# Kernel tuning notes

Hardware: AMD Instinct MI355X
Metric: run time of the kernel (lower is better)

## Reference

```python
import jax, jax.numpy as jnp
import numpy as np

H_IMG = 256; W_IMG = 256; C = 256
WIN = (16, 16); STRIPE = (32, 32); DF = 4; NH = 4
ASZ = (STRIPE[0] // DF, STRIPE[1] // DF)
TS = ((STRIPE[0] + ASZ[0]) // 2, (STRIPE[1] + ASZ[1]) // 2)  # stripe bias table half-size (20,20)


def _win_part(x, ws):
    # (B,H,W,c) -> (B*nW, ws0*ws1, c)
    B, H, W, c = x.shape
    x = x.reshape(B, H // ws[0], ws[0], W // ws[1], ws[1], c)
    return x.transpose(0, 1, 3, 2, 4, 5).reshape(-1, ws[0] * ws[1], c)


def _win_rev(w, ws, H, W):
    c = w.shape[-1]
    B = w.shape[0] // ((H // ws[0]) * (W // ws[1]))
    x = w.reshape(B, H // ws[0], W // ws[1], ws[0], ws[1], c)
    return x.transpose(0, 1, 3, 2, 4, 5).reshape(B, H, W, c)


def _l2n(x):
    # F.normalize(dim=-1)
    return x / jnp.maximum(jnp.linalg.norm(x, axis=-1, keepdims=True), 1e-12)


def _affine(attn, logit_scale, w1, b1, w2, table, index):
    # attn: (B_, nH, N1, N2); AffineTransform with mask=None
    N1, N2 = attn.shape[-2], attn.shape[-1]
    attn = attn * jnp.exp(jnp.minimum(logit_scale, np.log(100.0)))  # clamp max=log(1/0.01)
    bt = jax.nn.relu(table.reshape(-1, 2) @ w1 + b1) @ w2  # (T, nH)
    bias = bt[index.reshape(-1)].reshape(N1, N2, -1).transpose(2, 0, 1)  # (nH,N1,N2)
    return attn + (16.0 * jax.nn.sigmoid(bias))[None]


def _coords(start, size):
    h = np.arange(start[0], start[0] + size[0])
    w = np.arange(start[1], start[1] + size[1])
    return np.stack(np.meshgrid(h, w, indexing='ij')).reshape(2, -1)


def _idx(c1, c2, md):
    d = (c1[:, :, None] - c2[:, None, :]).transpose(1, 2, 0).astype(np.int64)
    return (d[..., 0] + md[0] - 1) * (2 * md[1] - 1) + (d[..., 1] + md[1] - 1)


def _table(ts):
    h = np.arange(-(ts[0] - 1), ts[0], dtype=np.float32) / (ts[0] - 1)
    w = np.arange(-(ts[1] - 1), ts[1], dtype=np.float32) / (ts[1] - 1)
    t = np.stack(np.meshgrid(h, w, indexing='ij'), axis=-1)[None] * 8.0
    return (np.sign(t) * np.log2(np.abs(t) + 1.0) / np.log2(8.0)).astype(np.float32)


def setup_inputs():
    ks = iter(jax.random.split(jax.random.key(0), 32))
    def nrm(shape, s=0.02):
        return jax.random.normal(next(ks), shape, dtype=jnp.float32) * s
    inp = {}
    inp['x'] = jax.random.normal(next(ks), (1, H_IMG * W_IMG, C), dtype=jnp.float32)
    inp['qkv_w'] = nrm((C, 3 * C)); inp['qkv_b'] = nrm((3 * C,))
    inp['anchor_w'] = nrm((C, C // 2)); inp['anchor_b'] = nrm((C // 2,))
    for tag in ['w', 's1', 's2']:
        inp['ls_' + tag] = jnp.full((NH, 1, 1), np.log(10.0), dtype=jnp.float32)
        inp['cpb_w1_' + tag] = nrm((2, 512), 0.1)
        inp['cpb_b1_' + tag] = nrm((512,), 0.1)
        inp['cpb_w2_' + tag] = nrm((512, NH), 0.1)
    inp['proj_w'] = nrm((C, C)); inp['proj_b'] = nrm((C,))
    inp['table_w'] = jnp.asarray(_table(WIN))
    inp['table_s'] = jnp.asarray(_table(TS))
    cw = _coords((0, 0), WIN)
    inp['index_w'] = jnp.asarray(_idx(cw, cw, WIN), dtype=jnp.int32)
    cs = _coords((0, 0), STRIPE)
    st = ((STRIPE[0] - ASZ[0]) // 2, (STRIPE[1] - ASZ[1]) // 2)
    ca = _coords(st, ASZ)
    inp['index_a2w'] = jnp.asarray(_idx(ca, cs, TS), dtype=jnp.int32)
    inp['index_w2a'] = jnp.asarray(_idx(cs, ca, TS), dtype=jnp.int32)
    return inp


def reference(x, qkv_w, qkv_b, anchor_w, anchor_b,
              ls_w, cpb_w1_w, cpb_b1_w, cpb_w2_w,
              ls_s1, cpb_w1_s1, cpb_b1_s1, cpb_w2_s1,
              ls_s2, cpb_w1_s2, cpb_b1_s2, cpb_w2_s2,
              proj_w, proj_b, table_w, table_s,
              index_w, index_a2w, index_w2a):
    B, L, c = x.shape
    qkv = x @ qkv_w + qkv_b               # (B, L, 3C)
    half = 3 * c // 2
    hd = half // 3 // NH                  # head_dim per branch
    # ---- window attention on first half of qkv channels ----
    qw = _win_part(qkv[..., :half].reshape(B, H_IMG, W_IMG, half), WIN)  # (B_, N, 3*C/2)
    B_, N, _ = qw.shape
    q, k, v = qw.reshape(B_, N, 3, NH, hd).transpose(2, 0, 3, 1, 4)
    attn = jnp.einsum('bhnd,bhmd->bhnm', _l2n(q), _l2n(k))
    attn = jax.nn.softmax(_affine(attn, ls_w, cpb_w1_w, cpb_b1_w, cpb_w2_w, table_w, index_w), axis=-1)
    xw = jnp.einsum('bhnm,bhmd->bhnd', attn, v).transpose(0, 2, 1, 3).reshape(B_, N, NH * hd)
    xw = _win_rev(xw, WIN, H_IMG, W_IMG).reshape(B, L, c // 2)
    # ---- anchor projection: AvgPool2d(DF) + Linear(C -> C/2) ----
    xi = x.reshape(B, H_IMG, W_IMG, c)
    pooled = xi.reshape(B, H_IMG // DF, DF, W_IMG // DF, DF, c).mean(axis=(2, 4))
    anchor = pooled @ anchor_w + anchor_b  # (B, H/DF, W/DF, C/2)
    # ---- anchor stripe attention on second half ----
    qs = _win_part(qkv[..., half:].reshape(B, H_IMG, W_IMG, half), STRIPE)  # (Bs, N1, 3*C/2)
    Bs, N1, _ = qs.shape
    anc = _win_part(anchor, ASZ)           # (Bs, N2, C/2)
    N2 = anc.shape[1]
    q, k, v = qs.reshape(Bs, N1, 3, NH, hd).transpose(2, 0, 3, 1, 4)
    anc = anc.reshape(Bs, N2, NH, hd).transpose(0, 2, 1, 3)
    a1 = jnp.einsum('bhnd,bhmd->bhnm', _l2n(anc), _l2n(k))   # (Bs,NH,N2,N1)
    a1 = jax.nn.softmax(_affine(a1, ls_s1, cpb_w1_s1, cpb_b1_s1, cpb_w2_s1, table_s, index_a2w), axis=-1)
    xm = jnp.einsum('bhnm,bhmd->bhnd', a1, v)                # (Bs,NH,N2,hd)
    a2 = jnp.einsum('bhnd,bhmd->bhnm', _l2n(q), _l2n(anc))   # (Bs,NH,N1,N2)
    a2 = jax.nn.softmax(_affine(a2, ls_s2, cpb_w1_s2, cpb_b1_s2, cpb_w2_s2, table_s, index_w2a), axis=-1)
    xs = jnp.einsum('bhnm,bhmd->bhnd', a2, xm).transpose(0, 2, 1, 3).reshape(Bs, N1, NH * hd)
    xs = _win_rev(xs, STRIPE, H_IMG, W_IMG).reshape(B, L, c // 2)
    # ---- merge + output projection ----
    return jnp.concatenate([xw, xs], axis=-1) @ proj_w + proj_b
```

## Files before the change

### kernel.cpp

```cpp
#include <hip/hip_runtime.h>
#include <cstdint>
#include <cstddef>

typedef unsigned short u16;
typedef __attribute__((ext_vector_type(8))) short short8;
typedef __attribute__((ext_vector_type(4))) float floatx4;
typedef __attribute__((ext_vector_type(2))) float floatx2;
typedef __attribute__((ext_vector_type(4))) unsigned int uintx4;
typedef __attribute__((ext_vector_type(2))) unsigned int uintx2;
typedef __attribute__((ext_vector_type(2))) __bf16 bf16x2;

#define LOG2E 1.44269504f

__device__ __forceinline__ float bf2f(u16 u){
  union { unsigned int i; float f; } v; v.i = ((unsigned int)u) << 16; return v.f;
}
__device__ __forceinline__ u16 f2bf(float f){
  union { __bf16 b; u16 u; } v; v.b = (__bf16)f; return v.u;
}
__device__ __forceinline__ unsigned int pk2(float a, float b){
  union { bf16x2 h; unsigned int u; } v;
  v.h = __builtin_convertvector((floatx2){a, b}, bf16x2);
  return v.u;
}
__device__ __forceinline__ void gload16(const void* g, void* l){
  __builtin_amdgcn_global_load_lds((const __attribute__((address_space(1))) unsigned int*)g,
                                   (__attribute__((address_space(3))) unsigned int*)l, 16, 0, 0);
}
__device__ __forceinline__ uintx4 ld8f_bf(const float* g){
  floatx4 u0 = *(const floatx4*)g;
  floatx4 u1 = *(const floatx4*)(g + 4);
  uintx4 w;
  w.x = pk2(u0.x, u0.y); w.y = pk2(u0.z, u0.w);
  w.z = pk2(u1.x, u1.y); w.w = pk2(u1.z, u1.w);
  return w;
}
__device__ __forceinline__ float redq(float v){
  v += __shfl_xor(v, 16); v += __shfl_xor(v, 32);
  return v;
}

__global__ void transpose_w(const float* __restrict__ qkv_w, const float* __restrict__ anchor_w,
                            const float* __restrict__ proj_w,
                            u16* __restrict__ qkvt, u16* __restrict__ anct, u16* __restrict__ projt){
  int id = blockIdx.x*256 + threadIdx.x;
  if (id < 196608){ int k = id / 768, n = id % 768; qkvt[n*256 + k] = f2bf(qkv_w[id]); }
  else if (id < 229376){ int r = id - 196608; int k = r / 128, n = r % 128; anct[n*256 + k] = f2bf(anchor_w[r]); }
  else { int r = id - 229376; int k = r >> 8, n = r & 255; projt[n*256 + k] = f2bf(proj_w[r]); }
}

__global__ void cpb_mlp(const float* __restrict__ tw, const float* __restrict__ ts,
                        const float* __restrict__ w1w, const float* __restrict__ b1w, const float* __restrict__ w2w,
                        const float* __restrict__ w1s1, const float* __restrict__ b1s1, const float* __restrict__ w2s1,
                        const float* __restrict__ w1s2, const float* __restrict__ b1s2, const float* __restrict__ w2s2,
                        float* __restrict__ btw, float* __restrict__ bts1, float* __restrict__ bts2){
  int tag = blockIdx.y;
  const float *tab, *w1, *b1, *w2; float* bt; int T;
  if (tag == 0){ tab = tw; w1 = w1w;  b1 = b1w;  w2 = w2w;  bt = btw;  T = 961; }
  else if (tag == 1){ tab = ts; w1 = w1s1; b1 = b1s1; w2 = w2s1; bt = bts1; T = 1521; }
  else { tab = ts; w1 = w1s2; b1 = b1s2; w2 = w2s2; bt = bts2; T = 1521; }
  __shared__ float sw1[2][512];
  __shared__ float sb1[512];
  __shared__ float sw2[512][4];
  for (int j = threadIdx.x; j < 512; j += 256){
    sw1[0][j] = w1[j]; sw1[1][j] = w1[512 + j]; sb1[j] = b1[j];
    for (int h = 0; h < 4; ++h) sw2[j][h] = w2[j*4 + h];
  }
  __syncthreads();
  int idx = blockIdx.x*256 + threadIdx.x;
  int r = idx >> 2, hh = idx & 3;
  if (r < T){
    float t0 = tab[2*r], t1 = tab[2*r + 1];
    float acc = 0.f;
    for (int j = 0; j < 512; ++j){
      float hj = fmaxf(fmaf(t0, sw1[0][j], fmaf(t1, sw1[1][j], sb1[j])), 0.f);
      acc = fmaf(hj, sw2[j][hh], acc);
    }
    bt[r*4 + hh] = acc;
  }
}

__global__ void bias_gather(const float* __restrict__ btw, const float* __restrict__ bts1,
                            const float* __restrict__ bts2,
                            const int* __restrict__ idxw, const int* __restrict__ idxa2w,
                            const int* __restrict__ idxw2a,
                            const float* __restrict__ lsw, const float* __restrict__ ls1,
                            const float* __restrict__ ls2,
                            float* __restrict__ bw, float* __restrict__ bs1, float* __restrict__ bs2){
  int id = blockIdx.x*256 + threadIdx.x;
  int which = id >> 18;
  int rem = id & 262143;
  int h = rem >> 16, e = rem & 65535;
  const float* bt; const int* ix; float* dst; const float* ls;
  if (which == 0){ bt = btw;  ix = idxw;   dst = bw;  ls = lsw; }
  else if (which == 1){ bt = bts1; ix = idxa2w; dst = bs1; ls = ls1; }
  else { bt = bts2; ix = idxw2a; dst = bs2; ls = ls2; }
  float v = bt[ix[e]*4 + h];
  float scale = exp2f(fminf(ls[h], 4.6051702f) * LOG2E);
  float off = fminf(scale + 16.f, 80.f);
  float sig = 16.f / (1.f + exp2f(-v * LOG2E));
  float out = (sig - off) * LOG2E;
  int idx;
  if (which == 0){
    int q = e >> 8, k = e & 255;
    idx = ((((h*8 + (k>>5))*2 + ((k>>4)&1))*4 + ((k>>2)&3)) << 10) + (q << 2) + (k & 3);
  } else if (which == 1){
    int a = e >> 10, k = e & 1023;
    idx = (((h*64 + (k>>4))*4 + ((k>>2)&3)) << 8) + (a << 2) + (k & 3);
  } else {
    int q = e >> 6, k = e & 63;
    idx = (((h*4 + (k>>4))*4 + ((k>>2)&3)) << 12) + (q << 2) + (k & 3);
  }
  dst[idx] = out;
}

__global__ void avgpool(const float* __restrict__ x, float* __restrict__ pooled){
  int a = blockIdx.x, c = threadIdx.x;
  int ay = a >> 6, ax = a & 63;
  float acc = 0.f;
#pragma unroll
  for (int dy = 0; dy < 4; ++dy)
#pragma unroll
    for (int dx = 0; dx < 4; ++dx)
      acc += x[(size_t)((ay*4 + dy)*256 + ax*4 + dx)*256 + c];
  pooled[(size_t)a*256 + c] = acc * 0.0625f;
}

__launch_bounds__(256, 2)
__global__ void gemm_qkv(const float* __restrict__ A, const u16* __restrict__ Bt,
                         const float* __restrict__ bias, u16* __restrict__ C,
                         int N, int K){
  __shared__ __align__(16) u16 lsA[4096];
  __shared__ __align__(16) u16 lsB[4096];
  const int tid = threadIdx.x, lane = tid & 63, wv = tid >> 6;
  const int lane15 = lane & 15, quad = lane >> 4;
  const int wr = wv >> 1, wc = wv & 1;
  const int m0 = blockIdx.x * 128;
  const int y = blockIdx.y;
  const u16* Btb = Bt + (size_t)y*128*K;
  const float* bb = bias + y*128;
  char* lsBb = (char*)lsB;
  const int brow = wv*16 + (lane >> 2);
  const u16* bsrc = Btb + (size_t)brow*K + (lane & 3)*8;
  const int arow = tid & 127, aq = tid >> 7;
  const float* asrc = A + (size_t)(m0 + arow)*K;
  const int aslot0 = aq*1024 + ((arow + aq*2) & 127)*8;
  const int aslot1 = (aq+2)*1024 + ((arow + (aq+2)*2) & 127)*8;
  floatx4 acc[4][4] = {};
  for (int k0 = 0; k0 < K; k0 += 32){
    gload16(bsrc + k0,                 lsBb + wv*1024);
    gload16(bsrc + (size_t)64*K + k0,  lsBb + 4096 + wv*1024);
    uintx4 ra0 = ld8f_bf(asrc + k0 + aq*8);
    uintx4 ra1 = ld8f_bf(asrc + k0 + (aq+2)*8);
    *(uintx4*)(lsA + aslot0) = ra0;
    *(uintx4*)(lsA + aslot1) = ra1;
    __syncthreads();
    short8 a[4], b[4];
#pragma unroll
    for (int i = 0; i < 4; ++i){
      int r = wr*64 + i*16 + lane15;
      a[i] = *(const short8*)(lsA + quad*1024 + ((r + quad*2) & 127)*8);
    }
#pragma unroll
    for (int j = 0; j < 4; ++j)
      b[j] = *(const short8*)(lsBb + (wc*64 + j*16 + lane15)*64 + quad*16);
#pragma unroll
    for (int i = 0; i < 4; ++i)
#pragma unroll
      for (int j = 0; j < 4; ++j)
        acc[i][j] = __builtin_amdgcn_mfma_f32_16x16x32_bf16(b[j], a[i], acc[i][j], 0, 0, 0);
    __syncthreads();
  }
#pragma unroll
  for (int j = 0; j < 4; ++j){
    floatx4 bz = *(const floatx4*)(bb + wc*64 + j*16 + quad*4);
#pragma unroll
    for (int i = 0; i < 4; ++i) acc[i][j] += bz;
  }
  if (y < 2){
#pragma unroll
    for (int i = 0; i < 4; ++i){
#pragma unroll
      for (int jp = 0; jp < 2; ++jp){
        floatx4 s2 = acc[i][jp*2]*acc[i][jp*2] + acc[i][jp*2+1]*acc[i][jp*2+1];
        float ss = (s2.x + s2.y) + (s2.z + s2.w);
        ss = redq(ss);
        float inv = 1.f / fmaxf(sqrtf(ss), 1e-12f);
        acc[i][jp*2]   *= inv;
        acc[i][jp*2+1] *= inv;
      }
    }
  }
#pragma unroll
  for (int i = 0; i < 4; ++i){
    int row = m0 + wr*64 + i*16 + lane15;
#pragma unroll
    for (int j = 0; j < 4; ++j){
      int colb = y*128 + wc*64 + j*16 + quad*4;
      uintx2 w;
      w.x = pk2(acc[i][j][0], acc[i][j][1]);
      w.y = pk2(acc[i][j][2], acc[i][j][3]);
      *(uintx2*)(C + (size_t)row*N + colb) = w;
    }
  }
}

__launch_bounds__(256, 2)
__global__ void gemm_proj_inplace(float* __restrict__ AC, const u16* __restrict__ Bt,
                                  const float* __restrict__ bias){
  __shared__ __align__(16) u16 lsA[4096];
  __shared__ __align__(16) u16 lsB[8192];
  const int tid = threadIdx.x, lane = tid & 63, wv = tid >> 6;
  const int lane15 = lane & 15, quad = lane >> 4;
  const int wr = wv >> 1, wc = wv & 1;
  const int m0 = blockIdx.x * 128;
  char* lsBb = (char*)lsB;
  const int brow = wv*16 + (lane >> 2);
  const u16* bsrc = Bt + (size_t)brow*256 + (lane & 3)*8;
  const int arow = tid & 127, aq = tid >> 7;
  const float* asrc = AC + (size_t)(m0 + arow)*256;
  const int aslot0 = aq*1024 + ((arow + aq*2) & 127)*8;
  const int aslot1 = (aq+2)*1024 + ((arow + (aq+2)*2) & 127)*8;
  floatx4 acc[4][8] = {};
  for (int k0 = 0; k0 < 256; k0 += 32){
    gload16(bsrc + k0,                lsBb +         wv*1024);
    gload16(bsrc + 64*256 + k0,       lsBb + 4096  + wv*1024);
    gload16(bsrc + 128*256 + k0,      lsBb + 8192  + wv*1024);
    gload16(bsrc + 192*256 + k0,      lsBb + 12288 + wv*1024);
    uintx4 ra0 = ld8f_bf(asrc + k0 + aq*8);
    uintx4 ra1 = ld8f_bf(asrc + k0 + (aq+2)*8);
    *(uintx4*)(lsA + aslot0) = ra0;
    *(uintx4*)(lsA + aslot1) = ra1;
    __syncthreads();
    short8 a[4], b[8];
#pragma unroll
    for (int i = 0; i < 4; ++i){
      int r = wr*64 + i*16 + lane15;
      a[i] = *(const short8*)(lsA + quad*1024 + ((r + quad*2) & 127)*8);
    }
#pragma unroll
    for (int j = 0; j < 8; ++j)
      b[j] = *(const short8*)(lsBb + (wc*128 + j*16 + lane15)*64 + quad*16);
#pragma unroll
    for (int i = 0; i < 4; ++i)
#pragma unroll
      for (int j = 0; j < 8; ++j)
        acc[i][j] = __builtin_amdgcn_mfma_f32_16x16x32_bf16(b[j], a[i], acc[i][j], 0, 0, 0);
    __syncthreads();
  }
#pragma unroll
  for (int i = 0; i < 4; ++i){
    int row = m0 + wr*64 + i*16 + lane15;
#pragma unroll
    for (int j = 0; j < 8; ++j){
      int colb = wc*128 + j*16 + quad*4;
      floatx4 bz = *(const floatx4*)(bias + colb);
      floatx4 o = acc[i][j] + bz;
      *(floatx4*)(AC + (size_t)row*256 + colb) = o;
    }
  }
}

__launch_bounds__(256, 3)
__global__ void win_attn(const u16* __restrict__ qkvh, const float* __restrict__ lsw,
                         const float* __restrict__ biasw, float* __restrict__ outm, int r0){
  __shared__ __align__(16) u16 sm[24576];
  const int tid = threadIdx.x, lane = tid & 63, wv = tid >> 6;
  const int lane15 = lane & 15, quad = lane >> 4;
  const int h = blockIdx.y;
  const int wyl = blockIdx.x >> 4, wx = blockIdx.x & 15;
  u16* Ks = sm;
  u16* Qs = sm + 8192;
  u16* VT = sm + 16384;
  {
    int tok = wv*64 + lane;
    int row = (wyl*16 + (tok >> 4))*256 + wx*16 + (tok & 15);
    const char* src = (const char*)qkvh + (size_t)row*768 + h*64;
#pragma unroll
    for (int kq = 0; kq < 4; ++kq){
      gload16(src + kq*16,        (char*)Qs + wv*1024 + kq*4096);
      gload16(src + 256 + kq*16,  (char*)Ks + wv*1024 + kq*4096);
    }
    int vrow = (wyl*16 + (tid >> 4))*256 + wx*16 + (tid & 15);
    const uintx4* vp = (const uintx4*)((const char*)qkvh + (size_t)vrow*768 + 512 + h*64);
    uintx4 v0 = vp[0], v1 = vp[1], v2 = vp[2], v3 = vp[3];
    unsigned int w[16] = {v0.x,v0.y,v0.z,v0.w, v1.x,v1.y,v1.z,v1.w,
                          v2.x,v2.y,v2.z,v2.w, v3.x,v3.y,v3.z,v3.w};
    u16* vd = VT + (tid >> 3)*256 + (tid & 7);
#pragma unroll
    for (int c = 0; c < 16; ++c){
      vd[(c*2)*8]   = (u16)(w[c] & 0xffffu);
      vd[(c*2+1)*8] = (u16)(w[c] >> 16);
    }
  }
  __syncthreads();
  short8 qf[4];
#pragma unroll
  for (int j = 0; j < 4; ++j)
    qf[j] = *(const short8*)(Qs + quad*2048 + (wv*64 + j*16 + lane15)*8);
  __syncthreads();

  float scale = exp2f(fminf(lsw[h], 4.6051702f) * LOG2E) * LOG2E;
  u16* Pw = Qs + wv*2048;
  const floatx4 zf4 = {0.f, 0.f, 0.f, 0.f};
  floatx4 accO[2][4] = {};
  float lsum[4] = {};

  for (int kc = 0; kc < 8; ++kc){
    floatx4 bia[2][4];
#pragma unroll
    for (int i = 0; i < 2; ++i)
#pragma unroll
      for (int j = 0; j < 4; ++j)
        bia[i][j] = *(const floatx4*)(biasw + ((((h*8 + kc)*2 + i)*4 + quad) << 10)
                                            + ((wv*64 + j*16 + lane15) << 2));
    short8 kf[2];
#pragma unroll
    for (int i = 0; i < 2; ++i)
      kf[i] = *(const short8*)(Ks + quad*2048 + (kc*32 + i*16 + lane15)*8);
#pragma unroll
    for (int i = 0; i < 2; ++i)
#pragma unroll
      for (int j = 0; j < 4; ++j){
        floatx4 sv = __builtin_amdgcn_mfma_f32_16x16x32_bf16(kf[i], qf[j], zf4, 0, 0, 0);
        float p0 = exp2f(fmaf(sv[0], scale, bia[i][j][0]));
        float p1 = exp2f(fmaf(sv[1], scale, bia[i][j][1]));
        float p2 = exp2f(fmaf(sv[2], scale, bia[i][j][2]));
        float p3 = exp2f(fmaf(sv[3], scale, bia[i][j][3]));
        lsum[j] += (p0 + p1) + (p2 + p3);
        uintx2 w; w.x = pk2(p0, p1); w.y = pk2(p2, p3);
        *(uintx2*)(Pw + (i*2 + (quad>>1))*512 + (j*16 + lane15)*8 + (quad&1)*4) = w;
      }
    asm volatile("s_waitcnt lgkmcnt(0)" ::: "memory");
    short8 ptf[4], vtf[2];
#pragma unroll
    for (int j = 0; j < 4; ++j)
      ptf[j] = *(const short8*)(Pw + quad*512 + (j*16 + lane15)*8);
#pragma unroll
    for (int m = 0; m < 2; ++m)
      vtf[m] = *(const short8*)(VT + (kc*4 + quad)*256 + (m*16 + lane15)*8);
#pragma unroll
    for (int m = 0; m < 2; ++m)
#pragma unroll
      for (int j = 0; j < 4; ++j)
        accO[m][j] = __builtin_amdgcn_mfma_f32_16x16x32_bf16(vtf[m], ptf[j], accO[m][j], 0, 0, 0);
  }
  float linv[4];
#pragma unroll
  for (int j = 0; j < 4; ++j) linv[j] = 1.f / redq(lsum[j]);
#pragma unroll
  for (int m = 0; m < 2; ++m)
#pragma unroll
    for (int j = 0; j < 4; ++j){
      int tok = wv*64 + j*16 + lane15;
      int py = r0 + wyl*16 + (tok >> 4), px = wx*16 + (tok & 15);
      floatx4 o = accO[m][j] * linv[j];
      *(floatx4*)(outm + (size_t)(py*256 + px)*256 + h*32 + m*16 + quad*4) = o;
    }
}

__launch_bounds__(256, 3)
__global__ void stripe_xm(const u16* __restrict__ qkvh, const u16* __restrict__ anchor,
                          const float* __restrict__ ls1, const float* __restrict__ bias1,
                          float* __restrict__ gl1, u16* __restrict__ gO, int r0){
  __shared__ __align__(16) u16 sm[22528];
  const int tid = threadIdx.x, lane = tid & 63, wv = tid >> 6;
  const int lane15 = lane & 15, quad = lane >> 4;
  const int s = blockIdx.x, h = blockIdx.y, kb = blockIdx.z;
  const int syl = s >> 3, sx = s & 7;
  u16* ANC = sm; u16* VT = sm + 10240; u16* P1T = sm + 14336;
  if (wv == 0){
    int ay = (r0 >> 2) + syl*8 + (lane >> 3), ax = sx*8 + (lane & 7);
    const char* asrc = (const char*)anchor + (size_t)(ay*64 + ax)*256 + h*64;
#pragma unroll
    for (int kq = 0; kq < 4; ++kq)
      gload16(asrc + kq*16, (char*)ANC + kq*1024);
  }
  auto stageK = [&](int kc){
    int kkb = kb*512 + kc*128;
    char* KC = (char*)sm + 4096 + (kc & 1)*8192;
#pragma unroll
    for (int hf = 0; hf < 2; ++hf){
      int tok = kkb + hf*64 + lane;
      int row = (syl*32 + (tok >> 5))*256 + sx*32 + (tok & 31);
      gload16((const char*)qkvh + (size_t)row*768 + 256 + h*64 + wv*16,
              KC + wv*2048 + hf*1024);
    }
  };
  stageK(0);
  float scale1 = exp2f(fminf(ls1[h], 4.6051702f) * LOG2E) * LOG2E;
  const floatx4 zf4 = {0.f, 0.f, 0.f, 0.f};
  floatx4 accO1[2] = {};
  float l1 = 0.f;
  for (int kc = 0; kc < 4; ++kc){
    int kkb = kb*512 + kc*128;
    {
      int tok_l = tid >> 1, dh = tid & 1;
      int tok = kkb + tok_l;
      int row = (syl*32 + (tok >> 5))*256 + sx*32 + (tok & 31);
      const uintx4* vp = (const uintx4*)((const char*)qkvh + (size_t)row*768 + 512 + h*64 + dh*32);
      uintx4 v0 = vp[0], v1 = vp[1];
      unsigned int w[8] = {v0.x,v0.y,v0.z,v0.w, v1.x,v1.y,v1.z,v1.w};
      u16* vd = VT + (tok_l >> 3)*256 + dh*128 + (tok_l & 7);
#pragma unroll
      for (int c = 0; c < 8; ++c){
        vd[(c*2)*8]   = (u16)(w[c] & 0xffffu);
        vd[(c*2+1)*8] = (u16)(w[c] >> 16);
      }
    }
    __syncthreads();
    if (kc < 3) stageK(kc + 1);
    const u16* KC = sm + 2048 + (kc & 1)*4096;
    short8 ancf = *(const short8*)(ANC + quad*512 + (wv*16 + lane15)*8);
    floatx4 bia[8];
#pragma unroll
    for (int i = 0; i < 8; ++i)
      bia[i] = *(const floatx4*)(bias1 + (((h*64 + kb*32 + kc*8 + i)*4 + quad) << 8)
                                       + ((wv*16 + lane15) << 2));
#pragma unroll
    for (int i = 0; i < 8; ++i){
      short8 kf = *(const short8*)(KC + quad*1024 + (i*16 + lane15)*8);
      floatx4 sv = __builtin_amdgcn_mfma_f32_16x16x32_bf16(kf, ancf, zf4, 0, 0, 0);
      float p0 = exp2f(fmaf(sv[0], scale1, bia[i][0]));
      float p1 = exp2f(fmaf(sv[1], scale1, bia[i][1]));
      float p2 = exp2f(fmaf(sv[2], scale1, bia[i][2]));
      float p3 = exp2f(fmaf(sv[3], scale1, bia[i][3]));
      l1 += (p0 + p1) + (p2 + p3);
      uintx2 w; w.x = pk2(p0, p1); w.y = pk2(p2, p3);
      *(uintx2*)(P1T + (i*2 + (quad>>1))*512 + (wv*16 + lane15)*8 + (quad&1)*4) = w;
    }
    asm volatile("s_waitcnt lgkmcnt(0)" ::: "memory");
#pragma unroll
    for (int ks = 0; ks < 4; ++ks){
      short8 ptf = *(const short8*)(P1T + (ks*4 + quad)*512 + (wv*16 + lane15)*8);
#pragma unroll
      for (int m = 0; m < 2; ++m){
        short8 vtf = *(const short8*)(VT + (ks*4 + quad)*256 + (m*16 + lane15)*8);
        accO1[m] = __builtin_amdgcn_mfma_f32_16x16x32_bf16(vtf, ptf, accO1[m], 0, 0, 0);
      }
    }
    __syncthreads();
  }
  l1 = redq(l1);
  int ent = (s*4 + h)*2 + kb;
  if (quad == 0) gl1[ent*64 + wv*16 + lane15] = l1;
#pragma unroll
  for (int m = 0; m < 2; ++m){
    uintx2 w; w.x = pk2(accO1[m][0], accO1[m][1]); w.y = pk2(accO1[m][2], accO1[m][3]);
    *(uintx2*)(gO + (size_t)ent*2048 + (wv*16 + lane15)*32 + m*16 + quad*4) = w;
  }
}

__launch_bounds__(256, 3)
__global__ void stripe_xs(const u16* __restrict__ qkvh, const u16* __restrict__ anchor,
                          const float* __restrict__ ls2, const float* __restrict__ bias2,
                          const float* __restrict__ gl1, const u16* __restrict__ gO,
                          float* __restrict__ outm, int r0){
  __shared__ __align__(16) u16 sm[20480];
  const int tid = threadIdx.x, lane = tid & 63, wv = tid >> 6;
  const int lane15 = lane & 15, quad = lane >> 4;
  const int s = blockIdx.x >> 2, qc = blockIdx.x & 3, h = blockIdx.y;
  const int syl = s >> 3, sx = s & 7;
  u16* ANC = sm;
  u16* XMT = sm + 2048;
  u16* QW  = sm + 4096 + wv*2048;
  u16* P2T = sm + 12288 + wv*2048;
  if (wv == 0){
    int ay = (r0 >> 2) + syl*8 + (lane >> 3), ax = sx*8 + (lane & 7);
    const char* asrc = (const char*)anchor + (size_t)(ay*64 + ax)*256 + h*64;
#pragma unroll
    for (int kq = 0; kq < 4; ++kq)
      gload16(asrc + kq*16, (char*)ANC + kq*1024);
  }
  {
    int a = tid >> 2, db = (tid & 3)*8;
    int e0 = (s*4 + h)*2;
    float inv = 1.f / (gl1[e0*64 + a] + gl1[(e0 + 1)*64 + a]);
    uintx4 u0 = *(const uintx4*)(gO + (size_t)e0*2048 + a*32 + db);
    uintx4 u1 = *(const uintx4*)(gO + (size_t)(e0 + 1)*2048 + a*32 + db);
    unsigned int w0[4] = {u0.x, u0.y, u0.z, u0.w};
    unsigned int w1[4] = {u1.x, u1.y, u1.z, u1.w};
#pragma unroll
    for (int c = 0; c < 4; ++c){
      float a0 = bf2f((u16)(w0[c] & 0xffffu)) + bf2f((u16)(w1[c] & 0xffffu));
      float a1 = bf2f((u16)(w0[c] >> 16))     + bf2f((u16)(w1[c] >> 16));
      XMT[(a >> 3)*256 + (db + c*2)*8     + (a & 7)] = f2bf(a0 * inv);
      XMT[(a >> 3)*256 + (db + c*2 + 1)*8 + (a & 7)] = f2bf(a1 * inv);
    }
  }
  int tq = qc*256 + wv*64;
  {
    int tok = tq + lane;
    int row = (syl*32 + (tok >> 5))*256 + sx*32 + (tok & 31);
    const char* src = (const char*)qkvh + (size_t)row*768 + h*64;
#pragma unroll
    for (int kq = 0; kq < 4; ++kq)
      gload16(src + kq*16, (char*)QW + kq*1024);
  }
  __syncthreads();
  short8 qf2[4];
#pragma unroll
  for (int j = 0; j < 4; ++j)
    qf2[j] = *(const short8*)(QW + quad*512 + (j*16 + lane15)*8);
  float scale2 = exp2f(fminf(ls2[h], 4.6051702f) * LOG2E) * LOG2E;
  const floatx4 zf4 = {0.f, 0.f, 0.f, 0.f};
  floatx4 accO2[2][4] = {};
  float l2[4] = {};
#pragma unroll
  for (int c = 0; c < 2; ++c){
    floatx4 bia[2][4];
#pragma unroll
    for (int i = 0; i < 2; ++i)
#pragma unroll
      for (int j = 0; j < 4; ++j)
        bia[i][j] = *(const floatx4*)(bias2 + ((((h*4 + c*2 + i)*4 + quad) << 12)
                                             + ((tq + j*16 + lane15) << 2)));
    short8 af[2];
#pragma unroll
    for (int i = 0; i < 2; ++i)
      af[i] = *(const short8*)(ANC + quad*512 + (c*32 + i*16 + lane15)*8);
#pragma unroll
    for (int i = 0; i < 2; ++i)
#pragma unroll
      for (int j = 0; j < 4; ++j){
        floatx4 sv = __builtin_amdgcn_mfma_f32_16x16x32_bf16(af[i], qf2[j], zf4, 0, 0, 0);
        float p0 = exp2f(fmaf(sv[0], scale2, bia[i][j][0]));
        float p1 = exp2f(fmaf(sv[1], scale2, bia[i][j][1]));
        float p2 = exp2f(fmaf(sv[2], scale2, bia[i][j][2]));
        float p3 = exp2f(fmaf(sv[3], scale2, bia[i][j][3]));
        l2[j] += (p0 + p1) + (p2 + p3);
        uintx2 w; w.x = pk2(p0, p1); w.y = pk2(p2, p3);
        *(uintx2*)(P2T + (i*2 + (quad>>1))*512 + (j*16 + lane15)*8 + (quad&1)*4) = w;
      }
    asm volatile("s_waitcnt lgkmcnt(0)" ::: "memory");
    short8 ptf[4], xmf[2];
#pragma unroll
    for (int j = 0; j < 4; ++j)
      ptf[j] = *(const short8*)(P2T + quad*512 + (j*16 + lane15)*8);
#pragma unroll
    for (int m = 0; m < 2; ++m)
      xmf[m] = *(const short8*)(XMT + (c*4 + quad)*256 + (m*16 + lane15)*8);
#pragma unroll
    for (int m = 0; m < 2; ++m)
#pragma unroll
      for (int j = 0; j < 4; ++j)
        accO2[m][j] = __builtin_amdgcn_mfma_f32_16x16x32_bf16(xmf[m], ptf[j], accO2[m][j], 0, 0, 0);
  }
  float linv[4];
#pragma unroll
  for (int j = 0; j < 4; ++j) linv[j] = 1.f / redq(l2[j]);
#pragma unroll
  for (int m = 0; m < 2; ++m)
#pragma unroll
    for (int j = 0; j < 4; ++j){
      int tok = tq + j*16 + lane15;
      int py = r0 + syl*32 + (tok >> 5), px = sx*32 + (tok & 31);
      floatx4 o = accO2[m][j] * linv[j];
      *(floatx4*)(outm + (size_t)(py*256 + px)*256 + 128 + h*32 + m*16 + quad*4) = o;
    }
}

extern "C" void kernel_launch(void* const* d_in, const int* in_sizes, int n_in,
                              void* d_out, int out_size, void* d_ws, size_t ws_size,
                              hipStream_t stream) {
  (void)in_sizes; (void)n_in; (void)out_size; (void)ws_size;
  const float* x        = (const float*)d_in[0];
  const float* qkv_w    = (const float*)d_in[1];
  const float* qkv_b    = (const float*)d_in[2];
  const float* anchor_w = (const float*)d_in[3];
  const float* anchor_b = (const float*)d_in[4];
  const float* ls_w     = (const float*)d_in[5];
  const float* w1_w     = (const float*)d_in[6];
  const float* b1_w     = (const float*)d_in[7];
  const float* w2_w     = (const float*)d_in[8];
  const float* ls_s1    = (const float*)d_in[9];
  const float* w1_s1    = (const float*)d_in[10];
  const float* b1_s1    = (const float*)d_in[11];
  const float* w2_s1    = (const float*)d_in[12];
  const float* ls_s2    = (const float*)d_in[13];
  const float* w1_s2    = (const float*)d_in[14];
  const float* b1_s2    = (const float*)d_in[15];
  const float* w2_s2    = (const float*)d_in[16];
  const float* proj_w   = (const float*)d_in[17];
  const float* proj_b   = (const float*)d_in[18];
  const float* table_w  = (const float*)d_in[19];
  const float* table_s  = (const float*)d_in[20];
  const int* index_w   = (const int*)d_in[21];
  const int* index_a2w = (const int*)d_in[22];
  const int* index_w2a = (const int*)d_in[23];

  char* ws = (char*)d_ws;
  u16*   qkvh   = (u16*)(ws + 0);
  float* pooled = (float*)(ws + 0);
  u16*   anch   = (u16*)(ws + 25165824);
  u16*   qkvt   = (u16*)(ws + 26214400);
  u16*   anct   = (u16*)(ws + 26607616);
  u16*   projt  = (u16*)(ws + 26673152);
  float* btw    = (float*)(ws + 26804224);
  float* bts1   = (float*)(ws + 26820608);
  float* bts2   = (float*)(ws + 26845184);
  float* biasw  = (float*)(ws + 26869760);
  float* bias1  = (float*)(ws + 27918336);
  float* bias2  = (float*)(ws + 28966912);
  float* gl1    = (float*)(ws + 30015488);
  u16*   gO     = (u16*)(ws + 30081024);

  float* merged = (float*)d_out;

  transpose_w<<<1152, 256, 0, stream>>>(qkv_w, anchor_w, proj_w, qkvt, anct, projt);
  cpb_mlp<<<dim3(24, 3), 256, 0, stream>>>(table_w, table_s,
                                           w1_w, b1_w, w2_w,
                                           w1_s1, b1_s1, w2_s1,
                                           w1_s2, b1_s2, w2_s2,
                                           btw, bts1, bts2);
  bias_gather<<<3072, 256, 0, stream>>>(btw, bts1, bts2, index_w, index_a2w, index_w2a,
                                        ls_w, ls_s1, ls_s2, biasw, bias1, bias2);
  avgpool<<<4096, 256, 0, stream>>>(x, pooled);
  gemm_qkv<<<dim3(32, 1), 256, 0, stream>>>(pooled, anct, anchor_b, anch, 128, 256);

  for (int half = 0; half < 2; ++half){
    const float* xh = x + (size_t)half*32768*256;
    int r0 = half*128;
    gemm_qkv<<<dim3(256, 3), 256, 0, stream>>>(xh, qkvt, qkv_b, qkvh, 384, 256);
    win_attn<<<dim3(128, 4), 256, 0, stream>>>(qkvh, ls_w, biasw, merged, r0);
    gemm_qkv<<<dim3(256, 3), 256, 0, stream>>>(xh, qkvt + 384*256, qkv_b + 384, qkvh, 384, 256);
    stripe_xm<<<dim3(32, 4, 2), 256, 0, stream>>>(qkvh, anch, ls_s1, bias1, gl1, gO, r0);
    stripe_xs<<<dim3(128, 4), 256, 0, stream>>>(qkvh, anch, ls_s2, bias2, gl1, gO, merged, r0);
  }

  gemm_proj_inplace<<<dim3(512), 256, 0, stream>>>(merged, projt, proj_b);
}
```

Measured before the change: 396.6 us.

## Fuse QKV column tiles per block, drop half-split, store merged bf16

The QKV GEMM now has each block stage its 128-row fp32 A tile once into LDS as bf16 and loop over all three 128-column output tiles, with double-buffered B loads. This removes the repeated A reads and conversions across blockIdx.y. The two image halves are processed in single full-size launches using separate workspace buffers for the window and stripe QKV. Attention outputs are written to a bf16 merged buffer, which the projection GEMM reads with async double-buffered loads instead of converting fp32 in place. The cost is more LDS per block (64KB for A), which may lower occupancy, plus a larger workspace footprint.

```diff
diff --git a/kernel.cpp b/kernel.cpp
--- a/kernel.cpp
+++ b/kernel.cpp
@@ -127,126 +127,133 @@
 }
 
 __launch_bounds__(256, 2)
-__global__ void gemm_qkv(const float* __restrict__ A, const u16* __restrict__ Bt,
-                         const float* __restrict__ bias, u16* __restrict__ C,
-                         int N, int K){
-  __shared__ __align__(16) u16 lsA[4096];
-  __shared__ __align__(16) u16 lsB[4096];
+__global__ void gemm_fused(const float* __restrict__ A, const u16* __restrict__ Bt,
+                           const float* __restrict__ bias, u16* __restrict__ C,
+                           int NY, int normY){
+  __shared__ __align__(16) u16 lsA[32768];
+  __shared__ __align__(16) u16 lsB[2][4096];
   const int tid = threadIdx.x, lane = tid & 63, wv = tid >> 6;
   const int lane15 = lane & 15, quad = lane >> 4;
   const int wr = wv >> 1, wc = wv & 1;
   const int m0 = blockIdx.x * 128;
-  const int y = blockIdx.y;
-  const u16* Btb = Bt + (size_t)y*128*K;
-  const float* bb = bias + y*128;
-  char* lsBb = (char*)lsB;
+  const int N = NY * 128;
   const int brow = wv*16 + (lane >> 2);
-  const u16* bsrc = Btb + (size_t)brow*K + (lane & 3)*8;
-  const int arow = tid & 127, aq = tid >> 7;
-  const float* asrc = A + (size_t)(m0 + arow)*K;
-  const int aslot0 = aq*1024 + ((arow + aq*2) & 127)*8;
-  const int aslot1 = (aq+2)*1024 + ((arow + (aq+2)*2) & 127)*8;
-  floatx4 acc[4][4] = {};
-  for (int k0 = 0; k0 < K; k0 += 32){
-    gload16(bsrc + k0,                 lsBb + wv*1024);
-    gload16(bsrc + (size_t)64*K + k0,  lsBb + 4096 + wv*1024);
-    uintx4 ra0 = ld8f_bf(asrc + k0 + aq*8);
-    uintx4 ra1 = ld8f_bf(asrc + k0 + (aq+2)*8);
-    *(uintx4*)(lsA + aslot0) = ra0;
-    *(uintx4*)(lsA + aslot1) = ra1;
-    __syncthreads();
-    short8 a[4], b[4];
+  const int bk = (lane & 3)*8;
+  auto stageB = [&](int y, int kw, int buf){
+    const u16* bs = Bt + (size_t)(y*128 + brow)*256 + kw*32 + bk;
+    char* d = (char*)lsB[buf];
+    gload16(bs,            d + wv*1024);
+    gload16(bs + 64*256,   d + 4096 + wv*1024);
+  };
+  stageB(0, 0, 0);
+  {
+    const int row = tid & 127, kh = tid >> 7;
+    const float* ap = A + (size_t)(m0 + row)*256 + kh*128;
+#pragma unroll
+    for (int i = 0; i < 16; ++i){
+      int k8 = kh*16 + i;
+      uintx4 w = ld8f_bf(ap + i*8);
+      *(uintx4*)(lsA + ((size_t)k8*128 + ((row + k8*2) & 127))*8) = w;
+    }
+  }
+  for (int y = 0; y < NY; ++y){
+    floatx4 acc[4][4] = {};
+    for (int kw = 0; kw < 8; ++kw){
+      const int it = y*8 + kw;
+      __syncthreads();
+      if (it + 1 < NY*8){
+        int nit = it + 1;
+        stageB(nit >> 3, nit & 7, nit & 1);
+      }
+      const char* Bc = (const char*)lsB[it & 1];
+      const int k8 = kw*4 + quad;
+      short8 a[4], b[4];
+#pragma unroll
+      for (int i = 0; i < 4; ++i)
+        a[i] = *(const short8*)(lsA + ((size_t)k8*128 + ((wr*64 + i*16 + lane15 + k8*2) & 127))*8);
+#pragma unroll
+      for (int j = 0; j < 4; ++j)
+        b[j] = *(const short8*)(Bc + (wc*64 + j*16 + lane15)*64 + quad*16);
+#pragma unroll
+      for (int i = 0; i < 4; ++i)
+#pragma unroll
+        for (int j = 0; j < 4; ++j)
+          acc[i][j] = __builtin_amdgcn_mfma_f32_16x16x32_bf16(b[j], a[i], acc[i][j], 0, 0, 0);
+    }
+#pragma unroll
+    for (int j = 0; j < 4; ++j){
+      floatx4 bz = *(const floatx4*)(bias + y*128 + wc*64 + j*16 + quad*4);
+#pragma unroll
+      for (int i = 0; i < 4; ++i) acc[i][j] += bz;
+    }
+    if (y < normY){
+#pragma unroll
+      for (int i = 0; i < 4; ++i)
+#pragma unroll
+        for (int jp = 0; jp < 2; ++jp){
+          floatx4 s2 = acc[i][jp*2]*acc[i][jp*2] + acc[i][jp*2+1]*acc[i][jp*2+1];
+          float ss = (s2.x + s2.y) + (s2.z + s2.w);
+          ss = redq(ss);
+          float inv = 1.f / fmaxf(sqrtf(ss), 1e-12f);
+          acc[i][jp*2]   *= inv;
+          acc[i][jp*2+1] *= inv;
+        }
+    }
 #pragma unroll
     for (int i = 0; i < 4; ++i){
-      int r = wr*64 + i*16 + lane15;
-      a[i] = *(const short8*)(lsA + quad*1024 + ((r + quad*2) & 127)*8);
-    }
-#pragma unroll
-    for (int j = 0; j < 4; ++j)
-      b[j] = *(const short8*)(lsBb + (wc*64 + j*16 + lane15)*64 + quad*16);
-#pragma unroll
-    for (int i = 0; i < 4; ++i)
-#pragma unroll
-      for (int j = 0; j < 4; ++j)
-        acc[i][j] = __builtin_amdgcn_mfma_f32_16x16x32_bf16(b[j], a[i], acc[i][j], 0, 0, 0);
-    __syncthreads();
-  }
-#pragma unroll
-  for (int j = 0; j < 4; ++j){
-    floatx4 bz = *(const floatx4*)(bb + wc*64 + j*16 + quad*4);
-#pragma unroll
-    for (int i = 0; i < 4; ++i) acc[i][j] += bz;
-  }
-  if (y < 2){
-#pragma unroll
-    for (int i = 0; i < 4; ++i){
-#pragma unroll
-      for (int jp = 0; jp < 2; ++jp){
-        floatx4 s2 = acc[i][jp*2]*acc[i][jp*2] + acc[i][jp*2+1]*acc[i][jp*2+1];
-        float ss = (s2.x + s2.y) + (s2.z + s2.w);
-        ss = redq(ss);
-        float inv = 1.f / fmaxf(sqrtf(ss), 1e-12f);
-        acc[i][jp*2]   *= inv;
-        acc[i][jp*2+1] *= inv;
+      int row = m0 + wr*64 + i*16 + lane15;
+#pragma unroll
+      for (int j = 0; j < 4; ++j){
+        int colb = y*128 + wc*64 + j*16 + quad*4;
+        uintx2 w;
+        w.x = pk2(acc[i][j][0], acc[i][j][1]);
+        w.y = pk2(acc[i][j][2], acc[i][j][3]);
+        *(uintx2*)(C + (size_t)row*N + colb) = w;
       }
     }
   }
-#pragma unroll
-  for (int i = 0; i < 4; ++i){
-    int row = m0 + wr*64 + i*16 + lane15;
-#pragma unroll
-    for (int j = 0; j < 4; ++j){
-      int colb = y*128 + wc*64 + j*16 + quad*4;
-      uintx2 w;
-      w.x = pk2(acc[i][j][0], acc[i][j][1]);
-      w.y = pk2(acc[i][j][2], acc[i][j][3]);
-      *(uintx2*)(C + (size_t)row*N + colb) = w;
-    }
-  }
 }
 
 __launch_bounds__(256, 2)
-__global__ void gemm_proj_inplace(float* __restrict__ AC, const u16* __restrict__ Bt,
-                                  const float* __restrict__ bias){
-  __shared__ __align__(16) u16 lsA[4096];
-  __shared__ __align__(16) u16 lsB[8192];
+__global__ void gemm_proj(const u16* __restrict__ Ab, const u16* __restrict__ Bt,
+                          const float* __restrict__ bias, float* __restrict__ Cout){
+  __shared__ __align__(16) u16 lsA[2][4096];
+  __shared__ __align__(16) u16 lsB[2][8192];
   const int tid = threadIdx.x, lane = tid & 63, wv = tid >> 6;
   const int lane15 = lane & 15, quad = lane >> 4;
   const int wr = wv >> 1, wc = wv & 1;
   const int m0 = blockIdx.x * 128;
-  char* lsBb = (char*)lsB;
-  const int brow = wv*16 + (lane >> 2);
-  const u16* bsrc = Bt + (size_t)brow*256 + (lane & 3)*8;
-  const int arow = tid & 127, aq = tid >> 7;
-  const float* asrc = AC + (size_t)(m0 + arow)*256;
-  const int aslot0 = aq*1024 + ((arow + aq*2) & 127)*8;
-  const int aslot1 = (aq+2)*1024 + ((arow + (aq+2)*2) & 127)*8;
+  const int srow = wv*16 + (lane >> 2), sk = (lane & 3)*8;
+  const u16* as = Ab + (size_t)(m0 + srow)*256 + sk;
+  const u16* bs = Bt + (size_t)srow*256 + sk;
+  auto stage = [&](int kw, int buf){
+    char* dA = (char*)lsA[buf]; char* dB = (char*)lsB[buf];
+    gload16(as + kw*32,             dA + wv*1024);
+    gload16(as + 64*256 + kw*32,    dA + 4096  + wv*1024);
+    gload16(bs + kw*32,             dB + wv*1024);
+    gload16(bs + 64*256 + kw*32,    dB + 4096  + wv*1024);
+    gload16(bs + 128*256 + kw*32,   dB + 8192  + wv*1024);
+    gload16(bs + 192*256 + kw*32,   dB + 12288 + wv*1024);
+  };
+  stage(0, 0);
   floatx4 acc[4][8] = {};
-  for (int k0 = 0; k0 < 256; k0 += 32){
-    gload16(bsrc + k0,                lsBb +         wv*1024);
-    gload16(bsrc + 64*256 + k0,       lsBb + 4096  + wv*1024);
-    gload16(bsrc + 128*256 + k0,      lsBb + 8192  + wv*1024);
-    gload16(bsrc + 192*256 + k0,      lsBb + 12288 + wv*1024);
-    uintx4 ra0 = ld8f_bf(asrc + k0 + aq*8);
-    uintx4 ra1 = ld8f_bf(asrc + k0 + (aq+2)*8);
-    *(uintx4*)(lsA + aslot0) = ra0;
-    *(uintx4*)(lsA + aslot1) = ra1;
+  for (int kw = 0; kw < 8; ++kw){
     __syncthreads();
+    if (kw < 7) stage(kw + 1, (kw + 1) & 1);
+    const char* Ac = (const char*)lsA[kw & 1];
+    const char* Bc = (const char*)lsB[kw & 1];
     short8 a[4], b[8];
 #pragma unroll
-    for (int i = 0; i < 4; ++i){
-      int r = wr*64 + i*16 + lane15;
-      a[i] = *(const short8*)(lsA + quad*1024 + ((r + quad*2) & 127)*8);
-    }
+    for (int i = 0; i < 4; ++i)
+      a[i] = *(const short8*)(Ac + (wr*64 + i*16 + lane15)*64 + quad*16);
 #pragma unroll
     for (int j = 0; j < 8; ++j)
-      b[j] = *(const short8*)(lsBb + (wc*128 + j*16 + lane15)*64 + quad*16);
+      b[j] = *(const short8*)(Bc + (wc*128 + j*16 + lane15)*64 + quad*16);
 #pragma unroll
     for (int i = 0; i < 4; ++i)
 #pragma unroll
       for (int j = 0; j < 8; ++j)
         acc[i][j] = __builtin_amdgcn_mfma_f32_16x16x32_bf16(b[j], a[i], acc[i][j], 0, 0, 0);
-    __syncthreads();
   }
 #pragma unroll
   for (int i = 0; i < 4; ++i){
@@ -256,14 +263,14 @@
       int colb = wc*128 + j*16 + quad*4;
       floatx4 bz = *(const floatx4*)(bias + colb);
       floatx4 o = acc[i][j] + bz;
-      *(floatx4*)(AC + (size_t)row*256 + colb) = o;
+      *(floatx4*)(Cout + (size_t)row*256 + colb) = o;
     }
   }
 }
 
 __launch_bounds__(256, 3)
 __global__ void win_attn(const u16* __restrict__ qkvh, const float* __restrict__ lsw,
-                         const float* __restrict__ biasw, float* __restrict__ outm, int r0){
+                         const float* __restrict__ biasw, u16* __restrict__ outm){
   __shared__ __align__(16) u16 sm[24576];
   const int tid = threadIdx.x, lane = tid & 63, wv = tid >> 6;
   const int lane15 = lane & 15, quad = lane >> 4;
@@ -353,16 +360,17 @@
 #pragma unroll
     for (int j = 0; j < 4; ++j){
       int tok = wv*64 + j*16 + lane15;
-      int py = r0 + wyl*16 + (tok >> 4), px = wx*16 + (tok & 15);
+      int py = wyl*16 + (tok >> 4), px = wx*16 + (tok & 15);
       floatx4 o = accO[m][j] * linv[j];
-      *(floatx4*)(outm + (size_t)(py*256 + px)*256 + h*32 + m*16 + quad*4) = o;
+      uintx2 w; w.x = pk2(o[0], o[1]); w.y = pk2(o[2], o[3]);
+      *(uintx2*)(outm + (size_t)(py*256 + px)*256 + h*32 + m*16 + quad*4) = w;
     }
 }
 
 __launch_bounds__(256, 3)
 __global__ void stripe_xm(const u16* __restrict__ qkvh, const u16* __restrict__ anchor,
                           const float* __restrict__ ls1, const float* __restrict__ bias1,
-                          float* __restrict__ gl1, u16* __restrict__ gO, int r0){
+                          float* __restrict__ gl1, u16* __restrict__ gO){
   __shared__ __align__(16) u16 sm[22528];
   const int tid = threadIdx.x, lane = tid & 63, wv = tid >> 6;
   const int lane15 = lane & 15, quad = lane >> 4;
@@ -370,7 +378,7 @@
   const int syl = s >> 3, sx = s & 7;
   u16* ANC = sm; u16* VT = sm + 10240; u16* P1T = sm + 14336;
   if (wv == 0){
-    int ay = (r0 >> 2) + syl*8 + (lane >> 3), ax = sx*8 + (lane & 7);
+    int ay = syl*8 + (lane >> 3), ax = sx*8 + (lane & 7);
     const char* asrc = (const char*)anchor + (size_t)(ay*64 + ax)*256 + h*64;
 #pragma unroll
     for (int kq = 0; kq < 4; ++kq)
@@ -455,7 +463,7 @@
 __global__ void stripe_xs(const u16* __restrict__ qkvh, const u16* __restrict__ anchor,
                           const float* __restrict__ ls2, const float* __restrict__ bias2,
                           const float* __restrict__ gl1, const u16* __restrict__ gO,
-                          float* __restrict__ outm, int r0){
+                          u16* __restrict__ outm){
   __shared__ __align__(16) u16 sm[20480];
   const int tid = threadIdx.x, lane = tid & 63, wv = tid >> 6;
   const int lane15 = lane & 15, quad = lane >> 4;
@@ -466,7 +474,7 @@
   u16* QW  = sm + 4096 + wv*2048;
   u16* P2T = sm + 12288 + wv*2048;
   if (wv == 0){
-    int ay = (r0 >> 2) + syl*8 + (lane >> 3), ax = sx*8 + (lane & 7);
+    int ay = syl*8 + (lane >> 3), ax = sx*8 + (lane & 7);
     const char* asrc = (const char*)anchor + (size_t)(ay*64 + ax)*256 + h*64;
 #pragma unroll
     for (int kq = 0; kq < 4; ++kq)
@@ -554,9 +562,10 @@
 #pragma unroll
     for (int j = 0; j < 4; ++j){
       int tok = tq + j*16 + lane15;
-      int py = r0 + syl*32 + (tok >> 5), px = sx*32 + (tok & 31);
+      int py = syl*32 + (tok >> 5), px = sx*32 + (tok & 31);
       floatx4 o = accO2[m][j] * linv[j];
-      *(floatx4*)(outm + (size_t)(py*256 + px)*256 + 128 + h*32 + m*16 + quad*4) = o;
+      uintx2 w; w.x = pk2(o[0], o[1]); w.y = pk2(o[2], o[3]);
+      *(uintx2*)(outm + (size_t)(py*256 + px)*256 + 128 + h*32 + m*16 + quad*4) = w;
     }
 }
 
@@ -590,22 +599,22 @@
   const int* index_w2a = (const int*)d_in[23];
 
   char* ws = (char*)d_ws;
-  u16*   qkvh   = (u16*)(ws + 0);
-  float* pooled = (float*)(ws + 0);
-  u16*   anch   = (u16*)(ws + 25165824);
-  u16*   qkvt   = (u16*)(ws + 26214400);
-  u16*   anct   = (u16*)(ws + 26607616);
-  u16*   projt  = (u16*)(ws + 26673152);
-  float* btw    = (float*)(ws + 26804224);
-  float* bts1   = (float*)(ws + 26820608);
-  float* bts2   = (float*)(ws + 26845184);
-  float* biasw  = (float*)(ws + 26869760);
-  float* bias1  = (float*)(ws + 27918336);
-  float* bias2  = (float*)(ws + 28966912);
-  float* gl1    = (float*)(ws + 30015488);
-  u16*   gO     = (u16*)(ws + 30081024);
-
-  float* merged = (float*)d_out;
+  u16*   qkvhW  = (u16*)(ws + 0);
+  u16*   qkvhS  = (u16*)(ws + 50331648);
+  u16*   mergedb= (u16*)(ws + 100663296);
+  float* pooled = (float*)(ws + 134217728);
+  u16*   anch   = (u16*)(ws + 138412032);
+  u16*   qkvt   = (u16*)(ws + 139460608);
+  u16*   anct   = (u16*)(ws + 139853824);
+  u16*   projt  = (u16*)(ws + 139919360);
+  float* btw    = (float*)(ws + 140050432);
+  float* bts1   = (float*)(ws + 140066816);
+  float* bts2   = (float*)(ws + 140091392);
+  float* biasw  = (float*)(ws + 140115968);
+  float* bias1  = (float*)(ws + 141164544);
+  float* bias2  = (float*)(ws + 142213120);
+  float* gl1    = (float*)(ws + 143261696);
+  u16*   gO     = (u16*)(ws + 143392768);
 
   transpose_w<<<1152, 256, 0, stream>>>(qkv_w, anchor_w, proj_w, qkvt, anct, projt);
   cpb_mlp<<<dim3(24, 3), 256, 0, stream>>>(table_w, table_s,
@@ -616,17 +625,11 @@
   bias_gather<<<3072, 256, 0, stream>>>(btw, bts1, bts2, index_w, index_a2w, index_w2a,
                                         ls_w, ls_s1, ls_s2, biasw, bias1, bias2);
   avgpool<<<4096, 256, 0, stream>>>(x, pooled);
-  gemm_qkv<<<dim3(32, 1), 256, 0, stream>>>(pooled, anct, anchor_b, anch, 128, 256);
-
-  for (int half = 0; half < 2; ++half){
-    const float* xh = x + (size_t)half*32768*256;
-    int r0 = half*128;
-    gemm_qkv<<<dim3(256, 3), 256, 0, stream>>>(xh, qkvt, qkv_b, qkvh, 384, 256);
-    win_attn<<<dim3(128, 4), 256, 0, stream>>>(qkvh, ls_w, biasw, merged, r0);
-    gemm_qkv<<<dim3(256, 3), 256, 0, stream>>>(xh, qkvt + 384*256, qkv_b + 384, qkvh, 384, 256);
-    stripe_xm<<<dim3(32, 4, 2), 256, 0, stream>>>(qkvh, anch, ls_s1, bias1, gl1, gO, r0);
-    stripe_xs<<<dim3(128, 4), 256, 0, stream>>>(qkvh, anch, ls_s2, bias2, gl1, gO, merged, r0);
-  }
-
-  gemm_proj_inplace<<<dim3(512), 256, 0, stream>>>(merged, projt, proj_b);
-}
+  gemm_fused<<<32, 256, 0, stream>>>(pooled, anct, anchor_b, anch, 1, 1);
+  gemm_fused<<<512, 256, 0, stream>>>(x, qkvt, qkv_b, qkvhW, 3, 2);
+  win_attn<<<dim3(256, 4), 256, 0, stream>>>(qkvhW, ls_w, biasw, mergedb);
+  gemm_fused<<<512, 256, 0, stream>>>(x, qkvt + 384*256, qkv_b + 384, qkvhS, 3, 2);
+  stripe_xm<<<dim3(64, 4, 2), 256, 0, stream>>>(qkvhS, anch, ls_s1, bias1, gl1, gO);
+  stripe_xs<<<dim3(256, 4), 256, 0, stream>>>(qkvhS, anch, ls_s2, bias2, gl1, gO, mergedb);
+  gemm_proj<<<512, 256, 0, stream>>>(mergedb, projt, proj_b, (float*)d_out);
+}
```

Result: faster. 351.2 us (-11.4%).
